# Kernel tuning notes

Measured on AMD Instinct MI355X. Metric: run time of the kernel, lower is better.

The kernel has to match this reference:

```python
import jax, jax.numpy as jnp
import numpy as np

B, N, D, U = 8, 2048, 512, 512

def setup_inputs() -> dict:
    key = jax.random.key(0)
    ks = jax.random.split(key, 7)
    s = 1.0 / np.sqrt(D)
    return {
        "inputs": jax.random.normal(ks[0], (B, N, D), dtype=jnp.float32),
        "Wq": jax.random.normal(ks[1], (D, U), dtype=jnp.float32) * s,
        "bq": jnp.zeros((U,), dtype=jnp.float32),
        "Wk": jax.random.normal(ks[2], (D, U), dtype=jnp.float32) * s,
        "bk": jnp.zeros((U,), dtype=jnp.float32),
        "Wv": jax.random.normal(ks[3], (D, U), dtype=jnp.float32) * s,
        "bv": jnp.zeros((U,), dtype=jnp.float32),
    }

def reference(inputs, Wq, bq, Wk, bk, Wv, bv):
    # Dense projections (Keras Dense: x @ W + b)
    Q = inputs @ Wq + bq  # [B, N, U]
    K = inputs @ Wk + bk  # [B, N, U]
    V = inputs @ Wv + bv  # [B, N, U]
    # NOTE: original module has NO 1/sqrt(d) scaling
    scores = jnp.einsum("bnu,bmu->bnm", Q, K)  # [B, N, N]
    attn = jax.nn.softmax(scores, axis=-1)
    return jnp.einsum("bnm,bmu->bnu", attn, V)  # [B, N, U]
```

## Files before the change

kernel.cpp:

```cpp
#include <hip/hip_runtime.h>


typedef _Float16 f16;
typedef _Float16 f16x4 __attribute__((ext_vector_type(4)));
typedef _Float16 f16x8 __attribute__((ext_vector_type(8)));
typedef float f32x4 __attribute__((ext_vector_type(4)));
typedef short s16x8 __attribute__((ext_vector_type(8)));
typedef unsigned short u16;

#define OFS 96.0f

__device__ __forceinline__ void stage16(const void* g, void* lds_uniform) {
    __builtin_amdgcn_global_load_lds(
        (const __attribute__((address_space(1))) void*)g,
        (__attribute__((address_space(3))) void*)lds_uniform,
        16, 0, 0);
}

__device__ __forceinline__ u16 f2bf(float f) {
    unsigned u = __builtin_bit_cast(unsigned, f);
    u = (u + 0x7FFF + ((u >> 16) & 1)) >> 16;
    return (u16)u;
}
__device__ __forceinline__ float bf2f(u16 b) {
    return __builtin_bit_cast(float, (unsigned)b << 16);
}

__global__ __launch_bounds__(256) void prep_fused(
    const float* __restrict__ X,
    const float* __restrict__ Wq, const float* __restrict__ Wk,
    const float* __restrict__ Wv,
    const float* __restrict__ bq, const float* __restrict__ bk,
    const float* __restrict__ bv,
    f16* __restrict__ X16, f16* __restrict__ Wt, float* __restrict__ biases,
    float* __restrict__ rowsum) {
    __shared__ float t[32][33];
    const int bid = blockIdx.x, tid = threadIdx.x;
    if (bid < 8192) {
        int i = (bid * 256 + tid) * 4;
        float4 v = *(const float4*)(X + i);
        f16x4 o;
        o[0] = (f16)v.x; o[1] = (f16)v.y; o[2] = (f16)v.z; o[3] = (f16)v.w;
        *(f16x4*)(X16 + i) = o;
    } else if (bid < 8960) {
        int id = bid - 8192;
        int z = id >> 8, rem = id & 255;
        int u0 = (rem & 15) * 32, d0 = (rem >> 4) * 32;
        const float* W = (z == 0) ? Wq : (z == 1 ? Wk : Wv);
        f16* outp = Wt + (size_t)z * 262144;
        int tx = tid & 31, ty = tid >> 5;
#pragma unroll
        for (int r = 0; r < 4; r++)
            t[ty + 8 * r][tx] = W[(size_t)(d0 + ty + 8 * r) * 512 + u0 + tx];
        __syncthreads();
#pragma unroll
        for (int r = 0; r < 4; r++)
            outp[(size_t)(u0 + ty + 8 * r) * 512 + d0 + tx] = (f16)t[tx][ty + 8 * r];
    } else if (bid == 8960) {
#pragma unroll
        for (int j = 0; j < 6; j++) {
            int i = j * 256 + tid;
            float v = (i < 512) ? bq[i] : (i < 1024) ? bk[i - 512] : bv[i - 1024];
            biases[i] = v;
        }
    } else {
        int id = bid - 8961;
        float4 z4 = {0.f, 0.f, 0.f, 0.f};
        ((float4*)rowsum)[id * 256 + tid] = z4;
    }
}

template <int MODE>
__device__ __forceinline__ void gemm_core(
    const u16* __restrict__ A, int lda,
    const u16* __restrict__ Bt, int ldb,
    int m0, int n0, int K,
    const float* __restrict__ bias, float* __restrict__ rs,
    void* __restrict__ Cv, int ldc,
    u16* As, u16* Bs) {
    __shared__ float rowbuf[128];

    const int tid = threadIdx.x;
    const int wid = tid >> 6, lane = tid & 63;

    if (MODE == 2 || MODE == 4) {
        if (tid < 128) rowbuf[tid] = (MODE == 2 ? bias : rs)[m0 + tid];
    }

    const int schunk = (lane & 7) ^ ((lane >> 3) & 7);
    const u16* gA = A + (size_t)(m0 + wid * 32 + (lane >> 3)) * lda + schunk * 8;
    const u16* gB = Bt + (size_t)(n0 + wid * 32 + (lane >> 3)) * ldb + schunk * 8;
    u16* ldsA = As + (wid * 32) * 64;
    u16* ldsB = Bs + (wid * 32) * 64;

    const int wr = wid >> 1, wc = wid & 1;
    const int frow = lane & 15;
    const int f7 = frow & 7;
    const int c_lo = (lane >> 4) ^ f7;
    const int c_hi = ((lane >> 4) | 4) ^ f7;
    const u16* fA_lo = As + (wr * 64 + frow) * 64 + c_lo * 8;
    const u16* fA_hi = As + (wr * 64 + frow) * 64 + c_hi * 8;
    const u16* fB_lo = Bs + (wc * 64 + frow) * 64 + c_lo * 8;
    const u16* fB_hi = Bs + (wc * 64 + frow) * 64 + c_hi * 8;

    f32x4 acc[4][4] = {};

    for (int kt = 0; kt < K; kt += 64) {
#pragma unroll
        for (int j = 0; j < 4; j++)
            stage16(gA + (size_t)(j * 8) * lda, ldsA + (j * 8) * 64);
#pragma unroll
        for (int j = 0; j < 4; j++)
            stage16(gB + (size_t)(j * 8) * ldb, ldsB + (j * 8) * 64);
        gA += 64; gB += 64;
        __syncthreads();

#pragma unroll
        for (int half = 0; half < 2; half++) {
            const u16* pA = half ? fA_hi : fA_lo;
            const u16* pB = half ? fB_hi : fB_lo;
            if (MODE == 4) {
                s16x8 af[4], bf[4];
#pragma unroll
                for (int i = 0; i < 4; i++) af[i] = *(const s16x8*)(pA + i * 16 * 64);
#pragma unroll
                for (int i = 0; i < 4; i++) bf[i] = *(const s16x8*)(pB + i * 16 * 64);
#pragma unroll
                for (int mi = 0; mi < 4; mi++)
#pragma unroll
                    for (int ni = 0; ni < 4; ni++)
                        acc[mi][ni] = __builtin_amdgcn_mfma_f32_16x16x32_bf16(
                            af[mi], bf[ni], acc[mi][ni], 0, 0, 0);
            } else {
                f16x8 af[4], bf[4];
#pragma unroll
                for (int i = 0; i < 4; i++) af[i] = *(const f16x8*)(const f16*)(pA + i * 16 * 64);
#pragma unroll
                for (int i = 0; i < 4; i++) bf[i] = *(const f16x8*)(const f16*)(pB + i * 16 * 64);
#pragma unroll
                for (int mi = 0; mi < 4; mi++)
#pragma unroll
                    for (int ni = 0; ni < 4; ni++)
                        acc[mi][ni] = __builtin_amdgcn_mfma_f32_16x16x32_f16(
                            af[mi], bf[ni], acc[mi][ni], 0, 0, 0);
            }
        }
        __syncthreads();
    }

    const int crow0 = m0 + wr * 64 + ((lane >> 4) << 2);
    const int ccol0 = n0 + wc * 64 + (lane & 15);

    if (MODE == 1) {
        f16* C = (f16*)Cv;
#pragma unroll
        for (int mi = 0; mi < 4; mi++)
#pragma unroll
            for (int ni = 0; ni < 4; ni++) {
                float cb = bias[ccol0 + ni * 16];
#pragma unroll
                for (int r = 0; r < 4; r++)
                    C[(size_t)(crow0 + mi * 16 + r) * ldc + ccol0 + ni * 16] =
                        (f16)(acc[mi][ni][r] + cb);
            }
    } else if (MODE == 2) {
        u16* C = (u16*)Cv;
#pragma unroll
        for (int mi = 0; mi < 4; mi++)
#pragma unroll
            for (int ni = 0; ni < 4; ni++)
#pragma unroll
                for (int r = 0; r < 4; r++) {
                    float rb = rowbuf[crow0 + mi * 16 + r - m0];
                    C[(size_t)(crow0 + mi * 16 + r) * ldc + ccol0 + ni * 16] =
                        f2bf(acc[mi][ni][r] + rb);
                }
    } else {
        float* C = (float*)Cv;
#pragma unroll
        for (int mi = 0; mi < 4; mi++) {
            float inv[4];
#pragma unroll
            for (int r = 0; r < 4; r++)
                inv[r] = 1.0f / rowbuf[crow0 + mi * 16 + r - m0];
#pragma unroll
            for (int ni = 0; ni < 4; ni++)
#pragma unroll
                for (int r = 0; r < 4; r++)
                    C[(size_t)(crow0 + mi * 16 + r) * ldc + ccol0 + ni * 16] =
                        acc[mi][ni][r] * inv[r];
        }
    }
}

__global__ __launch_bounds__(256) void proj_fused(
    const u16* __restrict__ X16, const u16* __restrict__ Wt,
    const float* __restrict__ biases,
    u16* __restrict__ QK, u16* __restrict__ Vt) {
    __shared__ __align__(16) u16 As[128 * 64];
    __shared__ __align__(16) u16 Bs[128 * 64];
    const int bid = blockIdx.x;
    if (bid < 1024) {
        int z = bid >> 9, rem = bid & 511;
        int bx = rem & 127, by = rem >> 7;
        gemm_core<1>(X16, 512, Wt + (size_t)z * 262144, 512,
                     bx * 128, by * 128, 512,
                     biases + z * 512, nullptr,
                     QK + (size_t)z * 8388608, 512, As, Bs);
    } else {
        int id = bid - 1024;
        int bz = id & 7, rem = id >> 3;
        int bx = rem & 3, by = rem >> 2;
        gemm_core<2>(Wt + (size_t)2 * 262144, 512,
                     X16 + (size_t)bz * 1048576, 512,
                     bx * 128, by * 128, 512,
                     biases + 1024, nullptr,
                     Vt + (size_t)bz * 1048576, 2048, As, Bs);
    }
}

__global__ __launch_bounds__(512, 2) void score_gemm(
    const u16* __restrict__ Q, const u16* __restrict__ Kk,
    u16* __restrict__ P, float* __restrict__ rowsum) {
    extern __shared__ __align__(16) char smem[];
    u16* As = (u16*)smem;
    u16* Bs = (u16*)(smem + 65536);

    const int i = blockIdx.x;
    const int z = i & 7, y = (i >> 3) & 7, x = i >> 6;
    const int m0 = x * 256, n0 = y * 256;
    const u16* A  = Q  + (size_t)z * 1048576;
    const u16* Bt = Kk + (size_t)z * 1048576;
    u16* C = P + (size_t)z * 4194304;
    float* rs = rowsum + z * 2048;

    const int tid = threadIdx.x;
    const int wid = tid >> 6, lane = tid & 63;

    const int srow = lane >> 3;
    const int schunk = (lane & 7) ^ srow;
    const u16* gA0 = A  + (size_t)m0 * 512 + schunk * 8;
    const u16* gB0 = Bt + (size_t)n0 * 512 + schunk * 8;
    const int w16 = wid * 16;
    const int baseU2 = w16 + (wid >= 4 ? 64 : 0);

    auto stage_unit = [&](int u, int T, int b) {
        int base = (u == 0) ? w16
                 : (u == 1) ? 128 + w16
                 : (u == 2) ? baseU2
                 : 64 + baseU2;
        const u16* g = (u < 2 ? gB0 : gA0) + (size_t)(base + srow) * 512 + T * 64;
        u16* l = (u < 2 ? Bs : As) + b * 16384 + base * 64;
        stage16(g, l);
        stage16(g + (size_t)8 * 512, l + 8 * 64);
    };

    const int wr = wid >> 2, wc = wid & 3;
    const int frow = lane & 15;
    const int f7 = frow & 7;
    const int c_lo = (lane >> 4) ^ f7;
    const int c_hi = ((lane >> 4) | 4) ^ f7;
    const int offB_lo = (wc * 64 + frow) * 64 + c_lo * 8;
    const int offB_hi = (wc * 64 + frow) * 64 + c_hi * 8;
    const int offA_lo = (wr * 128 + frow) * 64 + c_lo * 8;
    const int offA_hi = (wr * 128 + frow) * 64 + c_hi * 8;

    f32x4 acc[8][4] = {};

    stage_unit(0, 0, 0); stage_unit(1, 0, 0);
    stage_unit(2, 0, 0); stage_unit(3, 0, 0);
    stage_unit(0, 1, 1); stage_unit(1, 1, 1); stage_unit(2, 1, 1);
    asm volatile("s_waitcnt vmcnt(6)" ::: "memory");
    asm volatile("s_barrier" ::: "memory");

#pragma unroll 2
    for (int T = 0; T < 8; ++T) {
        const int buf = T & 1;
        const u16* Ab = As + buf * 16384;
        const u16* Bb = Bs + buf * 16384;

        f16x8 bf[4][2];
        {
#pragma unroll
            for (int ni = 0; ni < 4; ni++) {
                bf[ni][0] = *(const f16x8*)(const f16*)(Bb + offB_lo + ni * 16 * 64);
                bf[ni][1] = *(const f16x8*)(const f16*)(Bb + offB_hi + ni * 16 * 64);
            }
            f16x8 af[2][2];
#pragma unroll
            for (int m2 = 0; m2 < 2; m2++) {
                af[m2][0] = *(const f16x8*)(const f16*)(Ab + offA_lo + m2 * 16 * 64);
                af[m2][1] = *(const f16x8*)(const f16*)(Ab + offA_hi + m2 * 16 * 64);
            }
            if (T < 7) stage_unit(3, T + 1, buf ^ 1);
            asm volatile("s_barrier" ::: "memory");
            asm volatile("s_waitcnt lgkmcnt(0)" ::: "memory");
            __builtin_amdgcn_s_setprio(1);
#pragma unroll
            for (int kh = 0; kh < 2; kh++)
#pragma unroll
                for (int m2 = 0; m2 < 2; m2++)
#pragma unroll
                    for (int ni = 0; ni < 4; ni++)
                        acc[m2][ni] = __builtin_amdgcn_mfma_f32_16x16x32_f16(
                            af[m2][kh], bf[ni][kh], acc[m2][ni], 0, 0, 0);
            __builtin_amdgcn_s_setprio(0);
            asm volatile("s_barrier" ::: "memory");
        }
#pragma unroll
        for (int q = 1; q < 4; q++) {
            f16x8 af[2][2];
#pragma unroll
            for (int m2 = 0; m2 < 2; m2++) {
                af[m2][0] = *(const f16x8*)(const f16*)(Ab + offA_lo + (q * 2 + m2) * 16 * 64);
                af[m2][1] = *(const f16x8*)(const f16*)(Ab + offA_hi + (q * 2 + m2) * 16 * 64);
            }
            if (T < 6) stage_unit(q - 1, T + 2, buf);
            asm volatile("s_barrier" ::: "memory");
            asm volatile("s_waitcnt lgkmcnt(0)" ::: "memory");
            __builtin_amdgcn_s_setprio(1);
#pragma unroll
            for (int kh = 0; kh < 2; kh++)
#pragma unroll
                for (int m2 = 0; m2 < 2; m2++)
#pragma unroll
                    for (int ni = 0; ni < 4; ni++)
                        acc[q * 2 + m2][ni] = __builtin_amdgcn_mfma_f32_16x16x32_f16(
                            af[m2][kh], bf[ni][kh], acc[q * 2 + m2][ni], 0, 0, 0);
            __builtin_amdgcn_s_setprio(0);
            if (q == 3) {
                if (T < 6)       asm volatile("s_waitcnt vmcnt(6)" ::: "memory");
                else if (T == 6) asm volatile("s_waitcnt vmcnt(0)" ::: "memory");
            }
            asm volatile("s_barrier" ::: "memory");
        }
    }

    const int crow0 = m0 + wr * 128 + ((lane >> 4) << 2);
    const int ccol0 = n0 + wc * 64 + (lane & 15);
#pragma unroll
    for (int mi = 0; mi < 8; mi++)
#pragma unroll
        for (int r = 0; r < 4; r++) {
            float rsum = 0.0f;
#pragma unroll
            for (int ni = 0; ni < 4; ni++) {
                u16 b = f2bf(__expf(acc[mi][ni][r] - OFS));
                C[(size_t)(crow0 + mi * 16 + r) * 2048 + ccol0 + ni * 16] = b;
                rsum += bf2f(b);
            }
#pragma unroll
            for (int o = 1; o < 16; o <<= 1)
                rsum += __shfl_xor(rsum, o, 64);
            if ((lane & 15) == 0)
                atomicAdd(rs + crow0 + mi * 16 + r, rsum);
        }
}

__global__ __launch_bounds__(256) void pv_gemm(
    const u16* __restrict__ P, const u16* __restrict__ Vt,
    float* __restrict__ rowsum, float* __restrict__ out) {
    __shared__ __align__(16) u16 As[128 * 64];
    __shared__ __align__(16) u16 Bs[128 * 64];
    const int i = blockIdx.x;
    const int z = i & 7, y = (i >> 3) & 3, x = i >> 5;
    gemm_core<4>(P + (size_t)z * 4194304, 2048,
                 Vt + (size_t)z * 1048576, 2048,
                 x * 128, y * 128, 2048,
                 nullptr, rowsum + z * 2048,
                 out + (size_t)z * 1048576, 512, As, Bs);
}


extern "C" void kernel_launch(void* const* d_in, const int* in_sizes, int n_in,
                              void* d_out, int out_size, void* d_ws, size_t ws_size,
                              hipStream_t stream) {
    const float* X  = (const float*)d_in[0];
    const float* Wq = (const float*)d_in[1];
    const float* bq = (const float*)d_in[2];
    const float* Wk = (const float*)d_in[3];
    const float* bk = (const float*)d_in[4];
    const float* Wv = (const float*)d_in[5];
    const float* bv = (const float*)d_in[6];
    float* out = (float*)d_out;
    char* ws = (char*)d_ws;

    f16*   X16    = (f16*)ws;
    f16*   Wt     = (f16*)(ws + 16777216);
    float* biases = (float*)(ws + 18350080);
    u16*   QK     = (u16*)(ws + 18356224);
    u16*   Vt     = (u16*)(ws + 51910656);
    u16*   P      = (u16*)(ws + 68687872);
    float* rowsum = (float*)(ws + 135796736);

    static bool s_attr_done = false;
    if (!s_attr_done) {
        (void)hipFuncSetAttribute(reinterpret_cast<const void*>(score_gemm),
                                  hipFuncAttributeMaxDynamicSharedMemorySize,
                                  131072);
        s_attr_done = true;
    }

    prep_fused<<<8977, 256, 0, stream>>>(X, Wq, Wk, Wv, bq, bk, bv,
                                         X16, Wt, biases, rowsum);

    proj_fused<<<1536, 256, 0, stream>>>((const u16*)X16, (const u16*)Wt,
                                         biases, QK, Vt);

    score_gemm<<<512, 512, 131072, stream>>>(QK, QK + (size_t)8388608, P, rowsum);

    pv_gemm<<<512, 256, 0, stream>>>(P, Vt, rowsum, out);
}
```

Baseline: 220.4 us.

## Restructure score GEMM pipeline to one-stage-ahead staging with inline-asm LDS reads

Reworks the score_gemm main loop from a two-tile-ahead staged pipeline to simple double buffering. Each K-step is split into four phases ordered by k-half and m-half, with B fragments reused across the two m-halves. LDS reads now go through explicit ds_read_b128 inline asm, and a sched_barrier keeps the compiler from reordering around the MFMA block. The aim is fewer barriers per tile and cheaper LDS addressing, at the cost of a shallower prefetch distance that may expose global load latency. It also sets an occupancy hint of 3 blocks per CU on proj_fused.

```diff
diff --git a/kernel.cpp b/kernel.cpp
--- a/kernel.cpp
+++ b/kernel.cpp
@@ -15,6 +15,16 @@
         (const __attribute__((address_space(1))) void*)g,
         (__attribute__((address_space(3))) void*)lds_uniform,
         16, 0, 0);
+}
+
+__device__ __forceinline__ unsigned lds_off(const void* p) {
+    return (unsigned)(size_t)(const __attribute__((address_space(3))) void*)p;
+}
+
+__device__ __forceinline__ f16x8 dsread16(unsigned a) {
+    f16x8 r;
+    asm volatile("ds_read_b128 %0, %1" : "=v"(r) : "v"(a));
+    return r;
 }
 
 __device__ __forceinline__ u16 f2bf(float f) {
@@ -193,7 +203,7 @@
     }
 }
 
-__global__ __launch_bounds__(256) void proj_fused(
+__global__ __launch_bounds__(256, 3) void proj_fused(
     const u16* __restrict__ X16, const u16* __restrict__ Wt,
     const float* __restrict__ biases,
     u16* __restrict__ QK, u16* __restrict__ Vt) {
@@ -223,8 +233,6 @@
     const u16* __restrict__ Q, const u16* __restrict__ Kk,
     u16* __restrict__ P, float* __restrict__ rowsum) {
     extern __shared__ __align__(16) char smem[];
-    u16* As = (u16*)smem;
-    u16* Bs = (u16*)(smem + 65536);
 
     const int i = blockIdx.x;
     const int z = i & 7, y = (i >> 3) & 7, x = i >> 6;
@@ -241,18 +249,15 @@
     const int schunk = (lane & 7) ^ srow;
     const u16* gA0 = A  + (size_t)m0 * 512 + schunk * 8;
     const u16* gB0 = Bt + (size_t)n0 * 512 + schunk * 8;
-    const int w16 = wid * 16;
-    const int baseU2 = w16 + (wid >= 4 ? 64 : 0);
+    char* ldsbase = smem;
 
     auto stage_unit = [&](int u, int T, int b) {
-        int base = (u == 0) ? w16
-                 : (u == 1) ? 128 + w16
-                 : (u == 2) ? baseU2
-                 : 64 + baseU2;
-        const u16* g = (u < 2 ? gB0 : gA0) + (size_t)(base + srow) * 512 + T * 64;
-        u16* l = (u < 2 ? Bs : As) + b * 16384 + base * 64;
+        const u16* gm = (u < 2) ? gA0 : gB0;
+        int rbase = (u & 1) * 128 + wid * 16;
+        const u16* g = gm + (size_t)(rbase + srow) * 512 + T * 64;
+        char* l = ldsbase + ((u < 2) ? 0 : 65536) + b * 32768 + rbase * 128;
         stage16(g, l);
-        stage16(g + (size_t)8 * 512, l + 8 * 64);
+        stage16(g + (size_t)8 * 512, l + 8 * 128);
     };
 
     const int wr = wid >> 2, wc = wid & 3;
@@ -260,78 +265,59 @@
     const int f7 = frow & 7;
     const int c_lo = (lane >> 4) ^ f7;
     const int c_hi = ((lane >> 4) | 4) ^ f7;
-    const int offB_lo = (wc * 64 + frow) * 64 + c_lo * 8;
-    const int offB_hi = (wc * 64 + frow) * 64 + c_hi * 8;
-    const int offA_lo = (wr * 128 + frow) * 64 + c_lo * 8;
-    const int offA_hi = (wr * 128 + frow) * 64 + c_hi * 8;
+    const unsigned smemB = lds_off(smem);
+    const unsigned offA_lo = (unsigned)(((wr * 128 + frow) * 64 + c_lo * 8) * 2);
+    const unsigned offA_hi = (unsigned)(((wr * 128 + frow) * 64 + c_hi * 8) * 2);
+    const unsigned offB_lo = (unsigned)(((wc * 64 + frow) * 64 + c_lo * 8) * 2);
+    const unsigned offB_hi = (unsigned)(((wc * 64 + frow) * 64 + c_hi * 8) * 2);
 
     f32x4 acc[8][4] = {};
 
     stage_unit(0, 0, 0); stage_unit(1, 0, 0);
     stage_unit(2, 0, 0); stage_unit(3, 0, 0);
-    stage_unit(0, 1, 1); stage_unit(1, 1, 1); stage_unit(2, 1, 1);
-    asm volatile("s_waitcnt vmcnt(6)" ::: "memory");
+    asm volatile("s_waitcnt vmcnt(0)" ::: "memory");
     asm volatile("s_barrier" ::: "memory");
 
-#pragma unroll 2
+#pragma unroll
     for (int T = 0; T < 8; ++T) {
         const int buf = T & 1;
-        const u16* Ab = As + buf * 16384;
-        const u16* Bb = Bs + buf * 16384;
-
-        f16x8 bf[4][2];
-        {
-#pragma unroll
-            for (int ni = 0; ni < 4; ni++) {
-                bf[ni][0] = *(const f16x8*)(const f16*)(Bb + offB_lo + ni * 16 * 64);
-                bf[ni][1] = *(const f16x8*)(const f16*)(Bb + offB_hi + ni * 16 * 64);
-            }
-            f16x8 af[2][2];
-#pragma unroll
-            for (int m2 = 0; m2 < 2; m2++) {
-                af[m2][0] = *(const f16x8*)(const f16*)(Ab + offA_lo + m2 * 16 * 64);
-                af[m2][1] = *(const f16x8*)(const f16*)(Ab + offA_hi + m2 * 16 * 64);
-            }
-            if (T < 7) stage_unit(3, T + 1, buf ^ 1);
-            asm volatile("s_barrier" ::: "memory");
+        const unsigned baseA = smemB + (unsigned)(buf * 32768);
+        const unsigned baseB = smemB + 65536u + (unsigned)(buf * 32768);
+
+        f16x8 bf[4];
+#pragma unroll
+        for (int p = 0; p < 4; ++p) {
+            const int kh = p >> 1, mh = p & 1;
+            const unsigned aoff = baseA + (kh ? offA_hi : offA_lo);
+            if (mh == 0) {
+                const unsigned boff = baseB + (kh ? offB_hi : offB_lo);
+#pragma unroll
+                for (int ni = 0; ni < 4; ni++)
+                    bf[ni] = dsread16(boff + (unsigned)(ni * 2048));
+            }
+            f16x8 af[4];
+#pragma unroll
+            for (int j = 0; j < 4; j++)
+                af[j] = dsread16(aoff + (unsigned)((4 * mh + j) * 2048));
+
+            if (T < 7) {
+                if (p == 0) { stage_unit(0, T + 1, buf ^ 1); stage_unit(1, T + 1, buf ^ 1); }
+                if (p == 1) { stage_unit(2, T + 1, buf ^ 1); stage_unit(3, T + 1, buf ^ 1); }
+            }
+
             asm volatile("s_waitcnt lgkmcnt(0)" ::: "memory");
+            __builtin_amdgcn_sched_barrier(0);
             __builtin_amdgcn_s_setprio(1);
 #pragma unroll
-            for (int kh = 0; kh < 2; kh++)
-#pragma unroll
-                for (int m2 = 0; m2 < 2; m2++)
-#pragma unroll
-                    for (int ni = 0; ni < 4; ni++)
-                        acc[m2][ni] = __builtin_amdgcn_mfma_f32_16x16x32_f16(
-                            af[m2][kh], bf[ni][kh], acc[m2][ni], 0, 0, 0);
+            for (int j = 0; j < 4; j++)
+#pragma unroll
+                for (int ni = 0; ni < 4; ni++)
+                    acc[4 * mh + j][ni] = __builtin_amdgcn_mfma_f32_16x16x32_f16(
+                        af[j], bf[ni], acc[4 * mh + j][ni], 0, 0, 0);
             __builtin_amdgcn_s_setprio(0);
-            asm volatile("s_barrier" ::: "memory");
-        }
-#pragma unroll
-        for (int q = 1; q < 4; q++) {
-            f16x8 af[2][2];
-#pragma unroll
-            for (int m2 = 0; m2 < 2; m2++) {
-                af[m2][0] = *(const f16x8*)(const f16*)(Ab + offA_lo + (q * 2 + m2) * 16 * 64);
-                af[m2][1] = *(const f16x8*)(const f16*)(Ab + offA_hi + (q * 2 + m2) * 16 * 64);
-            }
-            if (T < 6) stage_unit(q - 1, T + 2, buf);
-            asm volatile("s_barrier" ::: "memory");
-            asm volatile("s_waitcnt lgkmcnt(0)" ::: "memory");
-            __builtin_amdgcn_s_setprio(1);
-#pragma unroll
-            for (int kh = 0; kh < 2; kh++)
-#pragma unroll
-                for (int m2 = 0; m2 < 2; m2++)
-#pragma unroll
-                    for (int ni = 0; ni < 4; ni++)
-                        acc[q * 2 + m2][ni] = __builtin_amdgcn_mfma_f32_16x16x32_f16(
-                            af[m2][kh], bf[ni][kh], acc[q * 2 + m2][ni], 0, 0, 0);
-            __builtin_amdgcn_s_setprio(0);
-            if (q == 3) {
-                if (T < 6)       asm volatile("s_waitcnt vmcnt(6)" ::: "memory");
-                else if (T == 6) asm volatile("s_waitcnt vmcnt(0)" ::: "memory");
-            }
+
+            if (p == 3)
+                asm volatile("s_waitcnt vmcnt(0)" ::: "memory");
             asm volatile("s_barrier" ::: "memory");
         }
     }
```

Result: faster. 208.8 us (-5.3%).
